# Optimization experiments

Hardware: AMD Instinct MI355X
Metric: run time of the kernel (lower is better)

The kernel has to match this reference:

```python
import jax, jax.numpy as jnp
import numpy as np

DIM = 768
N_HEADS = 12
HEAD_DIM = DIM // N_HEADS
BATCH = 2
SEQ = 4096


def setup_inputs() -> dict:
    key = jax.random.key(0)
    ks = jax.random.split(key, 9)
    s = 1.0 / np.sqrt(DIM)
    return {
        "x": jax.random.normal(ks[0], (BATCH, SEQ, DIM), dtype=jnp.float32),
        "Wq": jax.random.normal(ks[1], (DIM, DIM), dtype=jnp.float32) * s,
        "bq": jax.random.normal(ks[2], (DIM,), dtype=jnp.float32) * s,
        "Wk": jax.random.normal(ks[3], (DIM, DIM), dtype=jnp.float32) * s,
        "bk": jax.random.normal(ks[4], (DIM,), dtype=jnp.float32) * s,
        "Wv": jax.random.normal(ks[5], (DIM, DIM), dtype=jnp.float32) * s,
        "bv": jax.random.normal(ks[6], (DIM,), dtype=jnp.float32) * s,
        "Wo": jax.random.normal(ks[7], (DIM, DIM), dtype=jnp.float32) * s,
        "bo": jax.random.normal(ks[8], (DIM,), dtype=jnp.float32) * s,
    }


def reference(x, Wq, bq, Wk, bk, Wv, bv, Wo, bo):
    B, S, D = x.shape
    scale = 1.0 / np.sqrt(HEAD_DIM).astype(np.float32)
    # projections: [B,S,D] -> [B,H,S,Hd]
    def split_heads(t):
        return t.reshape(B, S, N_HEADS, HEAD_DIM).transpose(0, 2, 1, 3)
    q = split_heads(x @ Wq + bq)
    k = split_heads(x @ Wk + bk)
    v = split_heads(x @ Wv + bv)
    # full score matrix [B,H,S,S] as in the original (memory-bound)
    scores = jnp.einsum("bhqd,bhkd->bhqk", q, k) * scale
    attn = jax.nn.softmax(scores, axis=-1)
    out = jnp.einsum("bhqk,bhkd->bhqd", attn, v)
    out = out.transpose(0, 2, 1, 3).reshape(B, S, D)
    return out @ Wo + bo
```

## Files before the change

### kernel.cpp

```cpp
#include <hip/hip_runtime.h>
#include <hip/hip_bf16.h>
#include <math.h>

#define D_MODEL 768
#define NH 12
#define HD 64
#define BATCH 2
#define SEQ 4096
#define NROWS (BATCH * SEQ)

#define QSCALE 0.18033688011112042f

typedef __attribute__((ext_vector_type(8))) short short8;
typedef __attribute__((ext_vector_type(4))) short short4v;
typedef __attribute__((ext_vector_type(4))) float f32x4;
typedef __attribute__((ext_vector_type(16))) float f32x16;
typedef __attribute__((ext_vector_type(4))) unsigned int uint4v;

__device__ inline unsigned short f2bf(float f) {
    __hip_bfloat16 h = __float2bfloat16(f);
    return *reinterpret_cast<unsigned short*>(&h);
}

__device__ __forceinline__ unsigned int cvtpk_bf16(float lo, float hi) {
    unsigned int d;
    asm("v_cvt_pk_bf16_f32 %0, %1, %2" : "=v"(d) : "v"(lo), "v"(hi));
    return d;
}

__device__ __forceinline__ short8 u4_as_s8(uint4v u) {
    return *reinterpret_cast<short8*>(&u);
}

__device__ __forceinline__ void async_ld16(const unsigned short* g, unsigned short* l) {
    __builtin_amdgcn_global_load_lds(
        (const __attribute__((address_space(1))) void*)g,
        (__attribute__((address_space(3))) void*)l, 16, 0, 0);
}

__global__ __launch_bounds__(256) void convert_x_k(
    const float* __restrict__ x, unsigned short* __restrict__ xb)
{
    size_t i = ((size_t)blockIdx.x * 256 + threadIdx.x) * 8;
    float4 a = *(const float4*)(x + i);
    float4 b = *(const float4*)(x + i + 4);
    short8 o;
    o[0] = (short)f2bf(a.x); o[1] = (short)f2bf(a.y);
    o[2] = (short)f2bf(a.z); o[3] = (short)f2bf(a.w);
    o[4] = (short)f2bf(b.x); o[5] = (short)f2bf(b.y);
    o[6] = (short)f2bf(b.z); o[7] = (short)f2bf(b.w);
    *(short8*)(xb + i) = o;
}

__global__ __launch_bounds__(256) void convert_wt_k(
    const float* __restrict__ Wq, const float* __restrict__ Wk,
    const float* __restrict__ Wv, const float* __restrict__ Wo,
    unsigned short* __restrict__ wt)
{
    const float* W = (blockIdx.z == 0) ? Wq : (blockIdx.z == 1) ? Wk
                   : (blockIdx.z == 2) ? Wv : Wo;
    unsigned short* dst = wt + (size_t)blockIdx.z * D_MODEL * D_MODEL;
    __shared__ float tile[64][65];
    const int k0 = blockIdx.x * 64, n0 = blockIdx.y * 64;
    const int t = threadIdx.x;
    const int r = t >> 2, seg = t & 3;
    const float* src = W + (size_t)(k0 + r) * D_MODEL + n0 + seg * 16;
    #pragma unroll
    for (int i = 0; i < 4; ++i) {
        float4 v = *(const float4*)(src + i * 4);
        tile[r][seg * 16 + i * 4 + 0] = v.x;
        tile[r][seg * 16 + i * 4 + 1] = v.y;
        tile[r][seg * 16 + i * 4 + 2] = v.z;
        tile[r][seg * 16 + i * 4 + 3] = v.w;
    }
    __syncthreads();
    unsigned short* d = dst + (size_t)(n0 + r) * D_MODEL + k0 + seg * 16;
    short8 o0, o1;
    #pragma unroll
    for (int j = 0; j < 8; ++j) o0[j] = (short)f2bf(tile[seg * 16 + j][r]);
    #pragma unroll
    for (int j = 0; j < 8; ++j) o1[j] = (short)f2bf(tile[seg * 16 + 8 + j][r]);
    *(short8*)(d) = o0;
    *(short8*)(d + 8) = o1;
}

__global__ __launch_bounds__(256, 3) void qkv_fused_k(
    const unsigned short* __restrict__ xb,
    const unsigned short* __restrict__ wt,
    const float* __restrict__ bq, const float* __restrict__ bk,
    const float* __restrict__ bv,
    unsigned short* __restrict__ qb,
    unsigned short* __restrict__ kb,
    unsigned short* __restrict__ vtb)
{
    __shared__ unsigned short As[128][64];
    __shared__ unsigned short Bs[3][64][64];
    const int t = threadIdx.x;
    const int w = t >> 6, lane = t & 63, quad = lane >> 4, col = lane & 15;
    const int r0 = blockIdx.x * 128;
    const int c0 = blockIdx.y * 64;

    f32x4 acc[3][2][4] = {};

    for (int kk = 0; kk < D_MODEL; kk += 64) {
        __syncthreads();
        #pragma unroll
        for (int j = 0; j < 4; ++j) {
            int c = (w * 4 + j) * 64 + lane;
            async_ld16(xb + (size_t)(r0 + (c >> 3)) * D_MODEL + kk + (c & 7) * 8,
                       &As[0][0] + (size_t)c * 8);
        }
        #pragma unroll
        for (int z = 0; z < 3; ++z) {
            const unsigned short* Wt = wt + (size_t)z * D_MODEL * D_MODEL;
            #pragma unroll
            for (int j = 0; j < 2; ++j) {
                int c = (w * 2 + j) * 64 + lane;
                async_ld16(Wt + (size_t)(c0 + (c >> 3)) * D_MODEL + kk + (c & 7) * 8,
                           &Bs[z][0][0] + (size_t)c * 8);
            }
        }
        __syncthreads();
        #pragma unroll
        for (int ks = 0; ks < 2; ++ks) {
            short8 af[2];
            af[0] = *(const short8*)&As[w * 32 + col][ks * 32 + quad * 8];
            af[1] = *(const short8*)&As[w * 32 + 16 + col][ks * 32 + quad * 8];
            #pragma unroll
            for (int z = 0; z < 3; ++z) {
                short8 bf[4];
                #pragma unroll
                for (int nt = 0; nt < 4; ++nt)
                    bf[nt] = *(const short8*)&Bs[z][nt * 16 + col][ks * 32 + quad * 8];
                #pragma unroll
                for (int mt = 0; mt < 2; ++mt)
                    #pragma unroll
                    for (int nt = 0; nt < 4; ++nt)
                        acc[z][mt][nt] = __builtin_amdgcn_mfma_f32_16x16x32_bf16(
                            af[mt], bf[nt], acc[z][mt][nt], 0, 0, 0);
            }
        }
    }

    const int h = blockIdx.y;
    #pragma unroll
    for (int z = 0; z < 3; ++z) {
        const float* bias = (z == 0) ? bq : (z == 1) ? bk : bv;
        #pragma unroll
        for (int nt = 0; nt < 4; ++nt) {
            const float bv_ = bias[c0 + nt * 16 + col];
            const int hd = nt * 16 + col;
            #pragma unroll
            for (int mt = 0; mt < 2; ++mt) {
                #pragma unroll
                for (int reg = 0; reg < 4; ++reg) {
                    int r = r0 + w * 32 + mt * 16 + quad * 4 + reg;
                    int b = r >> 12, s = r & (SEQ - 1);
                    float val = acc[z][mt][nt][reg] + bv_;
                    size_t bh = (size_t)(b * NH + h);
                    if (z == 0)
                        qb[(bh * SEQ + s) * HD + hd] = f2bf(val * QSCALE);
                    else if (z == 1)
                        kb[(bh * SEQ + s) * HD + hd] = f2bf(val);
                    else
                        vtb[(bh * HD + hd) * SEQ + s] = f2bf(val);
                }
            }
        }
    }
}

#define GEMM_STAGE(AS, BS, APTR, BPTR, KK)                                   \
    {                                                                        \
        _Pragma("unroll")                                                    \
        for (int j = 0; j < 4; ++j) {                                        \
            int c = (w * 4 + j) * 64 + lane;                                 \
            async_ld16(APTR + (size_t)(r0 + (c >> 3)) * D_MODEL + (KK) + (c & 7) * 8, \
                       &AS[0][0] + (size_t)c * 8);                           \
        }                                                                    \
        _Pragma("unroll")                                                    \
        for (int j = 0; j < 2; ++j) {                                        \
            int c = (w * 2 + j) * 64 + lane;                                 \
            async_ld16(BPTR + (size_t)(c0 + (c >> 3)) * D_MODEL + (KK) + (c & 7) * 8, \
                       &BS[0][0] + (size_t)c * 8);                           \
        }                                                                    \
    }

#define GEMM_COMPUTE(AS, BS)                                                 \
    {                                                                        \
        _Pragma("unroll")                                                    \
        for (int ks = 0; ks < 2; ++ks) {                                     \
            short8 af[2], bf[4];                                             \
            af[0] = *(const short8*)&AS[w * 32 + col][ks * 32 + quad * 8];   \
            af[1] = *(const short8*)&AS[w * 32 + 16 + col][ks * 32 + quad * 8]; \
            _Pragma("unroll")                                                \
            for (int nt = 0; nt < 4; ++nt)                                   \
                bf[nt] = *(const short8*)&BS[nt * 16 + col][ks * 32 + quad * 8]; \
            _Pragma("unroll")                                                \
            for (int mt = 0; mt < 2; ++mt)                                   \
                _Pragma("unroll")                                            \
                for (int nt = 0; nt < 4; ++nt)                               \
                    acc[mt][nt] = __builtin_amdgcn_mfma_f32_16x16x32_bf16(   \
                        af[mt], bf[nt], acc[mt][nt], 0, 0, 0);               \
        }                                                                    \
    }

__global__ __launch_bounds__(256) void out_mfma_k(
    const unsigned short* __restrict__ ab,
    const unsigned short* __restrict__ wot,
    const float* __restrict__ bo,
    float* __restrict__ out)
{
    __shared__ unsigned short As0[128][64], As1[128][64];
    __shared__ unsigned short Bs0[64][64],  Bs1[64][64];
    const int t = threadIdx.x;
    const int w = t >> 6, lane = t & 63, quad = lane >> 4, col = lane & 15;
    const int r0 = blockIdx.x * 128;
    const int c0 = blockIdx.y * 64;

    f32x4 acc[2][4] = {};

    GEMM_STAGE(As0, Bs0, ab, wot, 0);
    __syncthreads();
    #pragma unroll
    for (int kp = 0; kp < 6; ++kp) {
        GEMM_STAGE(As1, Bs1, ab, wot, kp * 128 + 64);
        GEMM_COMPUTE(As0, Bs0);
        __syncthreads();
        if (kp < 5) GEMM_STAGE(As0, Bs0, ab, wot, kp * 128 + 128);
        GEMM_COMPUTE(As1, Bs1);
        __syncthreads();
    }

    #pragma unroll
    for (int nt = 0; nt < 4; ++nt) {
        const float bv_ = bo[c0 + nt * 16 + col];
        #pragma unroll
        for (int mt = 0; mt < 2; ++mt) {
            #pragma unroll
            for (int reg = 0; reg < 4; ++reg) {
                int r = r0 + w * 32 + mt * 16 + quad * 4 + reg;
                out[(size_t)r * D_MODEL + c0 + nt * 16 + col] = acc[mt][nt][reg] + bv_;
            }
        }
    }
}

__device__ __forceinline__ void softmax_pack(
    const f32x16& s, float& lsum, short8& pf0, short8& pf1)
{
    float p[16];
    #pragma unroll
    for (int r = 0; r < 16; ++r)
        p[r] = __builtin_amdgcn_exp2f(s[r]);
    lsum += (((p[0] + p[1]) + (p[2] + p[3])) + ((p[4] + p[5]) + (p[6] + p[7])))
          + (((p[8] + p[9]) + (p[10] + p[11])) + ((p[12] + p[13]) + (p[14] + p[15])));
    unsigned int c01 = cvtpk_bf16(p[0],  p[1]);
    unsigned int c45 = cvtpk_bf16(p[4],  p[5]);
    unsigned int c23 = cvtpk_bf16(p[2],  p[3]);
    unsigned int c67 = cvtpk_bf16(p[6],  p[7]);
    unsigned int c89 = cvtpk_bf16(p[8],  p[9]);
    unsigned int cCD = cvtpk_bf16(p[12], p[13]);
    unsigned int cAB = cvtpk_bf16(p[10], p[11]);
    unsigned int cEF = cvtpk_bf16(p[14], p[15]);
    auto r0 = __builtin_amdgcn_permlane32_swap((int)c01, (int)c45, false, false);
    auto r1 = __builtin_amdgcn_permlane32_swap((int)c23, (int)c67, false, false);
    auto r2 = __builtin_amdgcn_permlane32_swap((int)c89, (int)cCD, false, false);
    auto r3 = __builtin_amdgcn_permlane32_swap((int)cAB, (int)cEF, false, false);
    uint4v u0, u1;
    u0[0] = (unsigned int)r0[0]; u0[1] = (unsigned int)r1[0];
    u0[2] = (unsigned int)r0[1]; u0[3] = (unsigned int)r1[1];
    u1[0] = (unsigned int)r2[0]; u1[1] = (unsigned int)r3[0];
    u1[2] = (unsigned int)r2[1]; u1[3] = (unsigned int)r3[1];
    pf0 = u4_as_s8(u0);
    pf1 = u4_as_s8(u1);
}

__global__ __launch_bounds__(256) void flash_mfma_k(
    const unsigned short* __restrict__ qb,
    const unsigned short* __restrict__ kb,
    const unsigned short* __restrict__ vtb,
    unsigned short* __restrict__ ab)
{
    __shared__ unsigned short Ks[64][66];
    __shared__ unsigned short Vts[64][66];

    const int t = threadIdx.x;
    const int w = t >> 6, lane = t & 63;
    const int l31 = lane & 31, hi = lane >> 5;
    const int q0 = blockIdx.x * 128;
    const int h = blockIdx.y, b = blockIdx.z;
    const size_t bh = (size_t)b * NH + h;
    const unsigned short* qg = qb + bh * SEQ * HD;
    const unsigned short* kg = kb + bh * SEQ * HD;
    const unsigned short* vg = vtb + bh * HD * SEQ;

    short8 qf[4];
    {
        const unsigned short* src = qg + (size_t)(q0 + w * 32 + l31) * HD + hi * 8;
        #pragma unroll
        for (int ks = 0; ks < 4; ++ks)
            qf[ks] = *(const short8*)(src + ks * 16);
    }

    f32x16 oacc[2] = {};
    float lsum = 0.f;
    const int srow = lane, sseg = w;

    short8 kr0, kr1, vr0, vr1;
    {
        const unsigned short* kp = kg + (size_t)srow * HD + sseg * 16;
        kr0 = *(const short8*)(kp);
        kr1 = *(const short8*)(kp + 8);
        const unsigned short* vp = vg + (size_t)srow * SEQ + sseg * 16;
        vr0 = *(const short8*)(vp);
        vr1 = *(const short8*)(vp + 8);
    }

    for (int kt = 0; kt < SEQ; kt += 64) {
        __syncthreads();
        *(short8*)&Ks[srow][sseg * 16]      = kr0;
        *(short8*)&Ks[srow][sseg * 16 + 8]  = kr1;
        *(short8*)&Vts[srow][sseg * 16]     = vr0;
        *(short8*)&Vts[srow][sseg * 16 + 8] = vr1;
        if (kt + 64 < SEQ) {
            const unsigned short* kp = kg + (size_t)(kt + 64 + srow) * HD + sseg * 16;
            kr0 = *(const short8*)(kp);
            kr1 = *(const short8*)(kp + 8);
            const unsigned short* vp = vg + (size_t)srow * SEQ + kt + 64 + sseg * 16;
            vr0 = *(const short8*)(vp);
            vr1 = *(const short8*)(vp + 8);
        }
        __syncthreads();

        short8 pf[4];
        #pragma unroll
        for (int kti = 0; kti < 2; ++kti) {
            f32x16 s = {};
            __builtin_amdgcn_s_setprio(1);
            #pragma unroll
            for (int ks = 0; ks < 4; ++ks) {
                short8 kf = *(const short8*)&Ks[kti * 32 + l31][ks * 16 + hi * 8];
                s = __builtin_amdgcn_mfma_f32_32x32x16_bf16(kf, qf[ks], s, 0, 0, 0);
            }
            __builtin_amdgcn_s_setprio(0);
            softmax_pack(s, lsum, pf[kti * 2 + 0], pf[kti * 2 + 1]);
        }

        __builtin_amdgcn_s_setprio(1);
        #pragma unroll
        for (int ks = 0; ks < 4; ++ks) {
            short8 pfk = pf[ks];
            #pragma unroll
            for (int dt = 0; dt < 2; ++dt) {
                short8 vf = *(const short8*)&Vts[dt * 32 + l31][ks * 16 + hi * 8];
                oacc[dt] = __builtin_amdgcn_mfma_f32_32x32x16_bf16(
                    vf, pfk, oacc[dt], 0, 0, 0);
            }
        }
        __builtin_amdgcn_s_setprio(0);
    }

    lsum += __shfl_xor(lsum, 32);
    float inv = 1.0f / lsum;
    int s = q0 + w * 32 + l31;
    unsigned short* dst = ab + ((size_t)b * SEQ + s) * D_MODEL + h * HD;
    #pragma unroll
    for (int dt = 0; dt < 2; ++dt) {
        #pragma unroll
        for (int rq = 0; rq < 4; ++rq) {
            short4v o4;
            o4[0] = (short)f2bf(oacc[dt][rq * 4 + 0] * inv);
            o4[1] = (short)f2bf(oacc[dt][rq * 4 + 1] * inv);
            o4[2] = (short)f2bf(oacc[dt][rq * 4 + 2] * inv);
            o4[3] = (short)f2bf(oacc[dt][rq * 4 + 3] * inv);
            *(short4v*)(dst + dt * 32 + rq * 8 + hi * 4) = o4;
        }
    }
}

extern "C" void kernel_launch(void* const* d_in, const int* in_sizes, int n_in,
                              void* d_out, int out_size, void* d_ws, size_t ws_size,
                              hipStream_t stream)
{
    const float* x  = (const float*)d_in[0];
    const float* Wq = (const float*)d_in[1];
    const float* bq = (const float*)d_in[2];
    const float* Wk = (const float*)d_in[3];
    const float* bk = (const float*)d_in[4];
    const float* Wv = (const float*)d_in[5];
    const float* bv = (const float*)d_in[6];
    const float* Wo = (const float*)d_in[7];
    const float* bo = (const float*)d_in[8];
    float* out = (float*)d_out;

    const size_t n_x  = (size_t)NROWS * D_MODEL;
    const size_t n_w  = (size_t)D_MODEL * D_MODEL;
    unsigned short* xb  = (unsigned short*)d_ws;
    unsigned short* wt  = xb + n_x;
    unsigned short* qb  = wt + 4 * n_w;
    unsigned short* kb  = qb + n_x;
    unsigned short* vtb = kb + n_x;
    unsigned short* ab  = vtb + n_x;
    const size_t need = ((size_t)5 * n_x + 4 * n_w) * sizeof(unsigned short);
    if (ws_size < need) return;

    convert_x_k<<<dim3((int)(n_x / 2048)), 256, 0, stream>>>(x, xb);
    convert_wt_k<<<dim3(12, 12, 4), 256, 0, stream>>>(Wq, Wk, Wv, Wo, wt);
    qkv_fused_k<<<dim3(NROWS / 128, D_MODEL / 64), 256, 0, stream>>>(
        xb, wt, bq, bk, bv, qb, kb, vtb);
    flash_mfma_k<<<dim3(SEQ / 128, NH, BATCH), 256, 0, stream>>>(qb, kb, vtb, ab);
    out_mfma_k<<<dim3(NROWS / 128, D_MODEL / 64), 256, 0, stream>>>(
        ab, wt + 3 * n_w, bo, out);
}
```

Before: 281.5 us.

## Pre-swizzle K/V into MFMA fragment order and read directly from global

The QKV kernel now writes K and V^T in a blocked layout that matches the MFMA operand fragment order per 64-key tile. The flash kernel drops its LDS staging and both __syncthreads per tile, and each lane loads its K and V fragments with coalesced 16-byte global loads. The grid is flattened and remapped (bid&7)*96 + bid>>3 so blocks for the same head land together, aiming at L2 locality across XCDs. The cost is that all four waves now load the same K/V tile separately from global or L2, with no register prefetch across iterations, so load latency may be exposed.

```diff
diff --git a/kernel.cpp b/kernel.cpp
--- a/kernel.cpp
+++ b/kernel.cpp
@@ -158,12 +158,24 @@
                     int b = r >> 12, s = r & (SEQ - 1);
                     float val = acc[z][mt][nt][reg] + bv_;
                     size_t bh = (size_t)(b * NH + h);
-                    if (z == 0)
+                    size_t bhb = bh * (size_t)(SEQ * HD);
+                    if (z == 0) {
                         qb[(bh * SEQ + s) * HD + hd] = f2bf(val * QSCALE);
-                    else if (z == 1)
-                        kb[(bh * SEQ + s) * HD + hd] = f2bf(val);
-                    else
-                        vtb[(bh * HD + hd) * SEQ + s] = f2bf(val);
+                    } else if (z == 1) {
+                        size_t idx = bhb + (size_t)(s >> 6) * 4096
+                                   + (size_t)((s >> 5) & 1) * 2048
+                                   + (size_t)(hd >> 4) * 512
+                                   + (size_t)((hd >> 3) & 1) * 256
+                                   + (size_t)(s & 31) * 8 + (hd & 7);
+                        kb[idx] = f2bf(val);
+                    } else {
+                        size_t idx = bhb + (size_t)(s >> 6) * 4096
+                                   + (size_t)(hd >> 5) * 2048
+                                   + (size_t)((s >> 4) & 3) * 512
+                                   + (size_t)((s >> 3) & 1) * 256
+                                   + (size_t)(hd & 31) * 8 + (s & 7);
+                        vtb[idx] = f2bf(val);
+                    }
                 }
             }
         }
@@ -282,18 +294,18 @@
     const unsigned short* __restrict__ vtb,
     unsigned short* __restrict__ ab)
 {
-    __shared__ unsigned short Ks[64][66];
-    __shared__ unsigned short Vts[64][66];
-
     const int t = threadIdx.x;
     const int w = t >> 6, lane = t & 63;
     const int l31 = lane & 31, hi = lane >> 5;
-    const int q0 = blockIdx.x * 128;
-    const int h = blockIdx.y, b = blockIdx.z;
+    const int bid = blockIdx.x;
+    const int lid = (bid & 7) * 96 + (bid >> 3);
+    const int q0 = (lid & 31) * 128;
+    const int hb = lid >> 5;
+    const int h = hb % NH, b = hb / NH;
     const size_t bh = (size_t)b * NH + h;
     const unsigned short* qg = qb + bh * SEQ * HD;
-    const unsigned short* kg = kb + bh * SEQ * HD;
-    const unsigned short* vg = vtb + bh * HD * SEQ;
+    const unsigned short* kgt = kb + bh * (size_t)(SEQ * HD);
+    const unsigned short* vgt = vtb + bh * (size_t)(SEQ * HD);
 
     short8 qf[4];
     {
@@ -305,58 +317,49 @@
 
     f32x16 oacc[2] = {};
     float lsum = 0.f;
-    const int srow = lane, sseg = w;
-
-    short8 kr0, kr1, vr0, vr1;
-    {
-        const unsigned short* kp = kg + (size_t)srow * HD + sseg * 16;
-        kr0 = *(const short8*)(kp);
-        kr1 = *(const short8*)(kp + 8);
-        const unsigned short* vp = vg + (size_t)srow * SEQ + sseg * 16;
-        vr0 = *(const short8*)(vp);
-        vr1 = *(const short8*)(vp + 8);
-    }
-
-    for (int kt = 0; kt < SEQ; kt += 64) {
-        __syncthreads();
-        *(short8*)&Ks[srow][sseg * 16]      = kr0;
-        *(short8*)&Ks[srow][sseg * 16 + 8]  = kr1;
-        *(short8*)&Vts[srow][sseg * 16]     = vr0;
-        *(short8*)&Vts[srow][sseg * 16 + 8] = vr1;
-        if (kt + 64 < SEQ) {
-            const unsigned short* kp = kg + (size_t)(kt + 64 + srow) * HD + sseg * 16;
-            kr0 = *(const short8*)(kp);
-            kr1 = *(const short8*)(kp + 8);
-            const unsigned short* vp = vg + (size_t)srow * SEQ + kt + 64 + sseg * 16;
-            vr0 = *(const short8*)(vp);
-            vr1 = *(const short8*)(vp + 8);
-        }
-        __syncthreads();
+
+    for (int T = 0; T < SEQ / 64; ++T) {
+        const unsigned short* kT = kgt + (size_t)T * 4096 + (size_t)lane * 8;
+        const unsigned short* vT = vgt + (size_t)T * 4096 + (size_t)lane * 8;
+        short8 kf0 = *(const short8*)(kT);
+        short8 kf1 = *(const short8*)(kT + 512);
+        short8 kf2 = *(const short8*)(kT + 1024);
+        short8 kf3 = *(const short8*)(kT + 1536);
+        short8 kf4 = *(const short8*)(kT + 2048);
+        short8 kf5 = *(const short8*)(kT + 2560);
+        short8 kf6 = *(const short8*)(kT + 3072);
+        short8 kf7 = *(const short8*)(kT + 3584);
 
         short8 pf[4];
-        #pragma unroll
-        for (int kti = 0; kti < 2; ++kti) {
+        {
             f32x16 s = {};
             __builtin_amdgcn_s_setprio(1);
-            #pragma unroll
-            for (int ks = 0; ks < 4; ++ks) {
-                short8 kf = *(const short8*)&Ks[kti * 32 + l31][ks * 16 + hi * 8];
-                s = __builtin_amdgcn_mfma_f32_32x32x16_bf16(kf, qf[ks], s, 0, 0, 0);
-            }
+            s = __builtin_amdgcn_mfma_f32_32x32x16_bf16(kf0, qf[0], s, 0, 0, 0);
+            s = __builtin_amdgcn_mfma_f32_32x32x16_bf16(kf1, qf[1], s, 0, 0, 0);
+            s = __builtin_amdgcn_mfma_f32_32x32x16_bf16(kf2, qf[2], s, 0, 0, 0);
+            s = __builtin_amdgcn_mfma_f32_32x32x16_bf16(kf3, qf[3], s, 0, 0, 0);
             __builtin_amdgcn_s_setprio(0);
-            softmax_pack(s, lsum, pf[kti * 2 + 0], pf[kti * 2 + 1]);
+            softmax_pack(s, lsum, pf[0], pf[1]);
+        }
+        {
+            f32x16 s = {};
+            __builtin_amdgcn_s_setprio(1);
+            s = __builtin_amdgcn_mfma_f32_32x32x16_bf16(kf4, qf[0], s, 0, 0, 0);
+            s = __builtin_amdgcn_mfma_f32_32x32x16_bf16(kf5, qf[1], s, 0, 0, 0);
+            s = __builtin_amdgcn_mfma_f32_32x32x16_bf16(kf6, qf[2], s, 0, 0, 0);
+            s = __builtin_amdgcn_mfma_f32_32x32x16_bf16(kf7, qf[3], s, 0, 0, 0);
+            __builtin_amdgcn_s_setprio(0);
+            softmax_pack(s, lsum, pf[2], pf[3]);
         }
 
         __builtin_amdgcn_s_setprio(1);
         #pragma unroll
         for (int ks = 0; ks < 4; ++ks) {
             short8 pfk = pf[ks];
-            #pragma unroll
-            for (int dt = 0; dt < 2; ++dt) {
-                short8 vf = *(const short8*)&Vts[dt * 32 + l31][ks * 16 + hi * 8];
-                oacc[dt] = __builtin_amdgcn_mfma_f32_32x32x16_bf16(
-                    vf, pfk, oacc[dt], 0, 0, 0);
-            }
+            short8 vf0 = *(const short8*)(vT + (size_t)ks * 512);
+            oacc[0] = __builtin_amdgcn_mfma_f32_32x32x16_bf16(vf0, pfk, oacc[0], 0, 0, 0);
+            short8 vf1 = *(const short8*)(vT + (size_t)(4 + ks) * 512);
+            oacc[1] = __builtin_amdgcn_mfma_f32_32x32x16_bf16(vf1, pfk, oacc[1], 0, 0, 0);
         }
         __builtin_amdgcn_s_setprio(0);
     }
@@ -409,7 +412,8 @@
     convert_wt_k<<<dim3(12, 12, 4), 256, 0, stream>>>(Wq, Wk, Wv, Wo, wt);
     qkv_fused_k<<<dim3(NROWS / 128, D_MODEL / 64), 256, 0, stream>>>(
         xb, wt, bq, bk, bv, qb, kb, vtb);
-    flash_mfma_k<<<dim3(SEQ / 128, NH, BATCH), 256, 0, stream>>>(qb, kb, vtb, ab);
+    flash_mfma_k<<<dim3(SEQ / 128 * NH * BATCH), 256, 0, stream>>>(
+        qb, kb, vtb, ab);
     out_mfma_k<<<dim3(NROWS / 128, D_MODEL / 64), 256, 0, stream>>>(
         ab, wt + 3 * n_w, bo, out);
 }
```

After: 288.3 us. +2.4%, slower.
